# Kernel optimization log

Hardware: AMD Instinct MI355X
Metric: run time of the kernel (lower is better)

The kernel has to match this reference:

```python
import jax, jax.numpy as jnp
import numpy as np

N_NODES = 100000


def gcn_conv(x, W, b, src, dst, n_nodes):
    """PyG GCNConv: D^{-1/2} (A + I) D^{-1/2} X W + b (self loops added)."""
    xw = x @ W  # [N, F_out]
    # degree over A + I, counted on destination (col) side
    deg = jnp.zeros((n_nodes,), dtype=x.dtype).at[dst].add(1.0) + 1.0
    dinv = jax.lax.rsqrt(deg)  # deg >= 1, safe
    # edge messages with symmetric normalization
    coef = dinv[src] * dinv[dst]  # [E]
    msg = xw[src] * coef[:, None]  # [E, F_out]
    agg = jax.ops.segment_sum(msg, dst, num_segments=n_nodes)
    # self-loop contribution: dinv[i]^2 * xw[i]
    out = agg + xw * (dinv * dinv)[:, None]
    return out + b


def setup_inputs() -> dict:
    key = jax.random.key(0)
    k1, k2, k3, k4 = jax.random.split(key, 4)
    input_dim, hidden_dim, output_dim = 64, 64, 32
    n_edges = 1600000
    x = jax.random.normal(k1, (N_NODES, input_dim), dtype=jnp.float32)
    edge_index = jax.random.randint(k2, (2, n_edges), 0, N_NODES, dtype=jnp.int64)
    # Glorot-style init for GCN weights, zero bias (PyG default)
    s1 = (6.0 / (input_dim + hidden_dim)) ** 0.5
    s2 = (6.0 / (hidden_dim + output_dim)) ** 0.5
    W1 = jax.random.uniform(k3, (input_dim, hidden_dim), jnp.float32, -s1, s1)
    W2 = jax.random.uniform(k4, (hidden_dim, output_dim), jnp.float32, -s2, s2)
    b1 = jnp.zeros((hidden_dim,), jnp.float32)
    b2 = jnp.zeros((output_dim,), jnp.float32)
    return {"x": x, "edge_index": edge_index, "W1": W1, "b1": b1, "W2": W2, "b2": b2}


def reference(x, edge_index, W1, b1, W2, b2):
    src, dst = edge_index[0], edge_index[1]
    h = jax.nn.relu(gcn_conv(x, W1, b1, src, dst, N_NODES))
    return gcn_conv(h, W2, b2, src, dst, N_NODES)
```

## Files before the change

### kernel.cpp

```cpp
#include <hip/hip_runtime.h>
#include <hip/hip_fp16.h>

#define NPB   64
#define KMAX  1600
#define BCAP  1280
#define EPB   8192

typedef _Float16 f16x8 __attribute__((ext_vector_type(8)));
typedef float    f32x4 __attribute__((ext_vector_type(4)));

__global__ __launch_bounds__(256) void bucket_scatter(
    const int* __restrict__ src, const int* __restrict__ dst, int E, int K,
    int* __restrict__ bucket_fill, unsigned* __restrict__ bucket_edges) {
    __shared__ int hist[KMAX];
    __shared__ int base[KMAX];
    for (int i = threadIdx.x; i < K; i += 256) hist[i] = 0;
    __syncthreads();
    int e0 = blockIdx.x * EPB;
    int e1 = min(e0 + EPB, E);
    for (int e = e0 + threadIdx.x; e < e1; e += 256)
        atomicAdd(&hist[dst[e] >> 6], 1);
    __syncthreads();
    for (int b = threadIdx.x; b < K; b += 256) {
        int h = hist[b];
        base[b] = h ? atomicAdd(&bucket_fill[b], h) : 0;
    }
    __syncthreads();
    for (int e = e0 + threadIdx.x; e < e1; e += 256) {
        int d = dst[e];
        int bb = d >> 6;
        int pos = atomicAdd(&base[bb], 1);
        if (pos < BCAP)
            bucket_edges[(size_t)bb * BCAP + pos] =
                ((unsigned)(d & 63) << 17) | (unsigned)src[e];
    }
}

__global__ __launch_bounds__(256) void bucket_csr(
    const int* __restrict__ bucket_fill, const unsigned* __restrict__ bucket_edges,
    unsigned* __restrict__ csr, int* __restrict__ rowstart, int* __restrict__ deg,
    float* __restrict__ dinv, int N) {
    __shared__ unsigned list[BCAP];
    __shared__ int cnt[NPB], pref[NPB], cnt2[NPB];
    const int b = blockIdx.x;
    const int m = min(bucket_fill[b], BCAP);
    if (threadIdx.x < NPB) { cnt[threadIdx.x] = 0; cnt2[threadIdx.x] = 0; }
    __syncthreads();
    const unsigned* bep = bucket_edges + (size_t)b * BCAP;
    for (int e = threadIdx.x; e < m; e += 256) {
        unsigned pk = bep[e];
        list[e] = pk;
        atomicAdd(&cnt[pk >> 17], 1);
    }
    __syncthreads();
    if (threadIdx.x < 64) {
        int lane = threadIdx.x;
        int c = cnt[lane];
        int x = c;
        for (int d = 1; d < 64; d <<= 1) {
            int y = __shfl_up(x, d, 64);
            if (lane >= d) x += y;
        }
        pref[lane] = x - c;
        int g = b * NPB + lane;
        if (g < N) {
            deg[g] = c;
            rowstart[g] = b * BCAP + (x - c);
            dinv[g] = rsqrtf((float)c + 1.0f);
        }
    }
    __syncthreads();
    for (int e = threadIdx.x; e < m; e += 256) {
        unsigned pk = list[e];
        int dl = pk >> 17;
        int r = atomicAdd(&cnt2[dl], 1);
        csr[(size_t)b * BCAP + pref[dl] + r] = pk & 0x1FFFF;
    }
}

__global__ void wtrans_k(const float* __restrict__ W1, const float* __restrict__ W2,
                         __half* __restrict__ W1T, __half* __restrict__ W2T) {
    int t = threadIdx.x;
    for (int i = t; i < 64 * 64; i += 256) {
        int f = i >> 6, k = i & 63;
        W1T[i] = __float2half(W1[k * 64 + f]);
    }
    for (int i = t; i < 32 * 64; i += 256) {
        int f = i >> 6, k = i & 63;
        W2T[i] = __float2half(W2[k * 32 + f]);
    }
}

__global__ __launch_bounds__(256) void gemm1_mfma(
    const float* __restrict__ X, const __half* __restrict__ W1T,
    const float* __restrict__ dinv, __half* __restrict__ out, int N) {
    const int wave = threadIdx.x >> 6, lane = threadIdx.x & 63;
    const int r = lane & 15, q = lane >> 4;
    const int nb = blockIdx.x * 16;
    const int node = nb + r;
    const int col = wave * 16 + r;
    f32x4 acc = {0.f, 0.f, 0.f, 0.f};
#pragma unroll
    for (int kt = 0; kt < 2; ++kt) {
        const float4* xr = (const float4*)(X + (size_t)node * 64 + kt * 32 + q * 8);
        float4 p0 = xr[0], p1 = xr[1];
        f16x8 a;
        a[0] = (_Float16)p0.x; a[1] = (_Float16)p0.y; a[2] = (_Float16)p0.z; a[3] = (_Float16)p0.w;
        a[4] = (_Float16)p1.x; a[5] = (_Float16)p1.y; a[6] = (_Float16)p1.z; a[7] = (_Float16)p1.w;
        f16x8 b = *(const f16x8*)(W1T + (size_t)col * 64 + kt * 32 + q * 8);
        acc = __builtin_amdgcn_mfma_f32_16x16x32_f16(a, b, acc, 0, 0, 0);
    }
#pragma unroll
    for (int i = 0; i < 4; ++i) {
        int nd = nb + q * 4 + i;
        out[(size_t)nd * 64 + wave * 16 + r] = __float2half(acc[i] * dinv[nd]);
    }
}

__global__ __launch_bounds__(256) void gemm2_mfma(
    const __half* __restrict__ H, const __half* __restrict__ W2T,
    const float* __restrict__ dinv, __half* __restrict__ out, int N) {
    const int wave = threadIdx.x >> 6, lane = threadIdx.x & 63;
    const int r = lane & 15, q = lane >> 4;
    const int nb = blockIdx.x * 32 + (wave >> 1) * 16;
    const int cb = (wave & 1) * 16;
    const int node = nb + r;
    const int col = cb + r;
    f32x4 acc = {0.f, 0.f, 0.f, 0.f};
#pragma unroll
    for (int kt = 0; kt < 2; ++kt) {
        f16x8 a = *(const f16x8*)(H + (size_t)node * 64 + kt * 32 + q * 8);
        f16x8 b = *(const f16x8*)(W2T + (size_t)col * 64 + kt * 32 + q * 8);
        acc = __builtin_amdgcn_mfma_f32_16x16x32_f16(a, b, acc, 0, 0, 0);
    }
#pragma unroll
    for (int i = 0; i < 4; ++i) {
        int nd = nb + q * 4 + i;
        out[(size_t)nd * 32 + cb + r] = __float2half(acc[i] * dinv[nd]);
    }
}

template <int F, bool RELU, typename OT>
__global__ __launch_bounds__(256) void aggregate_h2(
    const __half* __restrict__ xws, const unsigned* __restrict__ csr,
    const int* __restrict__ rowstart, const int* __restrict__ deg,
    const float* __restrict__ dinv, const float* __restrict__ bias,
    OT* __restrict__ out, int n) {
    constexpr int LPN = F / 2;
    int t = blockIdx.x * 256 + threadIdx.x;
    int node = t / LPN;
    int fl = t % LPN;
    if (node >= n) return;
    int m = deg[node];
    const unsigned* cp = csr + rowstart[node];
    const __half2* tab = (const __half2*)xws;
    float2 acc = __half22float2(tab[(size_t)node * LPN + fl]);
    int e = 0;
    for (; e + 8 <= m; e += 8) {
        unsigned s0 = cp[e+0], s1 = cp[e+1], s2 = cp[e+2], s3 = cp[e+3];
        unsigned s4 = cp[e+4], s5 = cp[e+5], s6 = cp[e+6], s7 = cp[e+7];
        float2 a0 = __half22float2(tab[(size_t)s0 * LPN + fl]);
        float2 a1 = __half22float2(tab[(size_t)s1 * LPN + fl]);
        float2 a2 = __half22float2(tab[(size_t)s2 * LPN + fl]);
        float2 a3 = __half22float2(tab[(size_t)s3 * LPN + fl]);
        float2 a4 = __half22float2(tab[(size_t)s4 * LPN + fl]);
        float2 a5 = __half22float2(tab[(size_t)s5 * LPN + fl]);
        float2 a6 = __half22float2(tab[(size_t)s6 * LPN + fl]);
        float2 a7 = __half22float2(tab[(size_t)s7 * LPN + fl]);
        acc.x += ((a0.x + a1.x) + (a2.x + a3.x)) + ((a4.x + a5.x) + (a6.x + a7.x));
        acc.y += ((a0.y + a1.y) + (a2.y + a3.y)) + ((a4.y + a5.y) + (a6.y + a7.y));
    }
    for (; e < m; ++e) {
        float2 a = __half22float2(tab[(size_t)cp[e] * LPN + fl]);
        acc.x += a.x; acc.y += a.y;
    }
    float dn = dinv[node];
    float2 bf = ((const float2*)bias)[fl];
    float vx = acc.x * dn + bf.x;
    float vy = acc.y * dn + bf.y;
    if (RELU) { vx = fmaxf(vx, 0.f); vy = fmaxf(vy, 0.f); }
    if constexpr (sizeof(OT) == 4) {
        ((__half2*)out)[(size_t)node * LPN + fl] = __floats2half2_rn(vx, vy);
    } else {
        ((float2*)out)[(size_t)node * LPN + fl] = make_float2(vx, vy);
    }
}


extern "C" void kernel_launch(void* const* d_in, const int* in_sizes, int n_in,
                              void* d_out, int out_size, void* d_ws, size_t ws_size,
                              hipStream_t stream) {
    const float* x  = (const float*)d_in[0];
    const int*   ei = (const int*)d_in[1];
    const float* W1 = (const float*)d_in[2];
    const float* b1 = (const float*)d_in[3];
    const float* W2 = (const float*)d_in[4];
    const float* b2 = (const float*)d_in[5];
    float* out = (float*)d_out;

    const int N = in_sizes[0] / 64;
    const int E = in_sizes[1] / 2;
    const int K = (N + NPB - 1) / NPB;
    const int* src = ei;
    const int* dst = ei + E;

    unsigned* be    = (unsigned*)d_ws;
    unsigned* csr   = be + (size_t)K * BCAP;
    int*      bfill = (int*)(csr + (size_t)K * BCAP);
    int*      rowst = bfill + K;
    int*      deg   = rowst + N;
    float*    dinv  = (float*)(deg + N);
    __half*   xws   = (__half*)(dinv + N);
    __half*   h     = xws + (size_t)N * 64;
    __half*   hw2   = h + (size_t)N * 64;
    __half*   W1T   = hw2 + (size_t)N * 32;
    __half*   W2T   = W1T + 64 * 64;

    hipMemsetAsync(bfill, 0, (size_t)K * sizeof(int), stream);

    int sb = (E + EPB - 1) / EPB;
    bucket_scatter<<<sb, 256, 0, stream>>>(src, dst, E, K, bfill, be);
    wtrans_k<<<1, 256, 0, stream>>>(W1, W2, W1T, W2T);
    bucket_csr<<<K, 256, 0, stream>>>(bfill, be, csr, rowst, deg, dinv, N);

    gemm1_mfma<<<N / 16, 256, 0, stream>>>(x, W1T, dinv, xws, N);
    aggregate_h2<64, true, __half2><<<(N * 32 + 255) / 256, 256, 0, stream>>>(
        xws, csr, rowst, deg, dinv, b1, (__half2*)h, N);
    gemm2_mfma<<<N / 32, 256, 0, stream>>>(h, W2T, dinv, hw2, N);
    aggregate_h2<32, false, float2><<<(N * 16 + 255) / 256, 256, 0, stream>>>(
        hw2, csr, rowst, deg, dinv, b2, (float2*)out, N);
}
```

Before: 250.8 us.

## Locally sort edges in shared memory before bucket scatter; pad CSR rows to 8

The bucket scatter kernel now counting-sorts each block's edges by bucket in shared memory and then writes them to global memory in contiguous runs, rather than issuing scattered per-edge writes. The CSR rows are padded to multiples of 8 with a dummy index that points at an extra zero row in the feature tables, so the aggregate loop no longer needs a scalar tail. In exchange it uses much more shared memory per scatter block (about 48KB), which lowers occupancy, and the padding adds wasted gathers from the zero row.

```diff
diff --git a/kernel.cpp b/kernel.cpp
--- a/kernel.cpp
+++ b/kernel.cpp
@@ -3,7 +3,8 @@
 
 #define NPB   64
 #define KMAX  1600
-#define BCAP  1280
+#define BCAP  1408
+#define CCAP  1920
 #define EPB   8192
 
 typedef _Float16 f16x8 __attribute__((ext_vector_type(8)));
@@ -13,33 +14,60 @@
     const int* __restrict__ src, const int* __restrict__ dst, int E, int K,
     int* __restrict__ bucket_fill, unsigned* __restrict__ bucket_edges) {
     __shared__ int hist[KMAX];
-    __shared__ int base[KMAX];
-    for (int i = threadIdx.x; i < K; i += 256) hist[i] = 0;
-    __syncthreads();
-    int e0 = blockIdx.x * EPB;
-    int e1 = min(e0 + EPB, E);
-    for (int e = e0 + threadIdx.x; e < e1; e += 256)
-        atomicAdd(&hist[dst[e] >> 6], 1);
-    __syncthreads();
-    for (int b = threadIdx.x; b < K; b += 256) {
-        int h = hist[b];
-        base[b] = h ? atomicAdd(&bucket_fill[b], h) : 0;
-    }
-    __syncthreads();
-    for (int e = e0 + threadIdx.x; e < e1; e += 256) {
-        int d = dst[e];
-        int bb = d >> 6;
-        int pos = atomicAdd(&base[bb], 1);
-        if (pos < BCAP)
-            bucket_edges[(size_t)bb * BCAP + pos] =
-                ((unsigned)(d & 63) << 17) | (unsigned)src[e];
+    __shared__ int lbase[KMAX];
+    __shared__ int gbase[KMAX];
+    __shared__ unsigned sorted[EPB];
+    __shared__ unsigned short bid[EPB];
+    __shared__ int wsum[4];
+    const int t = threadIdx.x;
+    for (int i = t; i < K; i += 256) hist[i] = 0;
+    __syncthreads();
+    const int e0 = blockIdx.x * EPB;
+    const int m = min(EPB, E - e0);
+    for (int e = t; e < m; e += 256) atomicAdd(&hist[dst[e0 + e] >> 6], 1);
+    __syncthreads();
+    constexpr int CH = (KMAX + 255) / 256;
+    int c[CH]; int s = 0;
+#pragma unroll
+    for (int j = 0; j < CH; ++j) { int idx = t * CH + j; c[j] = (idx < K) ? hist[idx] : 0; s += c[j]; }
+    int lane = t & 63, w = t >> 6;
+    int x = s;
+    for (int d = 1; d < 64; d <<= 1) { int y = __shfl_up(x, d, 64); if (lane >= d) x += y; }
+    if (lane == 63) wsum[w] = x;
+    __syncthreads();
+    int run = x - s;
+    for (int j = 0; j < 4; ++j) if (j < w) run += wsum[j];
+#pragma unroll
+    for (int j = 0; j < CH; ++j) {
+        int idx = t * CH + j;
+        if (idx < K) {
+            lbase[idx] = run;
+            if (c[j] > 0) gbase[idx] = atomicAdd(&bucket_fill[idx], c[j]);
+            run += c[j];
+        }
+    }
+    __syncthreads();
+    for (int i = t; i < K; i += 256) hist[i] = 0;
+    __syncthreads();
+    for (int e = t; e < m; e += 256) {
+        int d = dst[e0 + e], b = d >> 6;
+        int r = atomicAdd(&hist[b], 1);
+        int pos = lbase[b] + r;
+        sorted[pos] = ((unsigned)(d & 63) << 17) | (unsigned)src[e0 + e];
+        bid[pos] = (unsigned short)b;
+    }
+    __syncthreads();
+    for (int i = t; i < m; i += 256) {
+        int b = bid[i];
+        int off = gbase[b] + (i - lbase[b]);
+        if (off < BCAP) bucket_edges[(size_t)b * BCAP + off] = sorted[i];
     }
 }
 
 __global__ __launch_bounds__(256) void bucket_csr(
     const int* __restrict__ bucket_fill, const unsigned* __restrict__ bucket_edges,
     unsigned* __restrict__ csr, int* __restrict__ rowstart, int* __restrict__ deg,
-    float* __restrict__ dinv, int N) {
+    float* __restrict__ dinv, int N, unsigned PAD) {
     __shared__ unsigned list[BCAP];
     __shared__ int cnt[NPB], pref[NPB], cnt2[NPB];
     const int b = blockIdx.x;
@@ -56,17 +84,23 @@
     if (threadIdx.x < 64) {
         int lane = threadIdx.x;
         int c = cnt[lane];
-        int x = c;
+        int cpad = (c + 7) & ~7;
+        int x = cpad;
         for (int d = 1; d < 64; d <<= 1) {
             int y = __shfl_up(x, d, 64);
             if (lane >= d) x += y;
         }
-        pref[lane] = x - c;
+        int ex = x - cpad;
+        pref[lane] = ex;
         int g = b * NPB + lane;
         if (g < N) {
             deg[g] = c;
-            rowstart[g] = b * BCAP + (x - c);
+            rowstart[g] = b * CCAP + ex;
             dinv[g] = rsqrtf((float)c + 1.0f);
+        }
+        for (int p = c; p < cpad; ++p) {
+            int ci = ex + p;
+            if (ci < CCAP) csr[(size_t)b * CCAP + ci] = PAD;
         }
     }
     __syncthreads();
@@ -74,7 +108,8 @@
         unsigned pk = list[e];
         int dl = pk >> 17;
         int r = atomicAdd(&cnt2[dl], 1);
-        csr[(size_t)b * BCAP + pref[dl] + r] = pk & 0x1FFFF;
+        int ci = pref[dl] + r;
+        if (ci < CCAP) csr[(size_t)b * CCAP + ci] = pk & 0x1FFFF;
     }
 }
 
@@ -151,12 +186,11 @@
     int node = t / LPN;
     int fl = t % LPN;
     if (node >= n) return;
-    int m = deg[node];
+    int mp = (deg[node] + 7) & ~7;
     const unsigned* cp = csr + rowstart[node];
     const __half2* tab = (const __half2*)xws;
     float2 acc = __half22float2(tab[(size_t)node * LPN + fl]);
-    int e = 0;
-    for (; e + 8 <= m; e += 8) {
+    for (int e = 0; e < mp; e += 8) {
         unsigned s0 = cp[e+0], s1 = cp[e+1], s2 = cp[e+2], s3 = cp[e+3];
         unsigned s4 = cp[e+4], s5 = cp[e+5], s6 = cp[e+6], s7 = cp[e+7];
         float2 a0 = __half22float2(tab[(size_t)s0 * LPN + fl]);
@@ -170,10 +204,6 @@
         acc.x += ((a0.x + a1.x) + (a2.x + a3.x)) + ((a4.x + a5.x) + (a6.x + a7.x));
         acc.y += ((a0.y + a1.y) + (a2.y + a3.y)) + ((a4.y + a5.y) + (a6.y + a7.y));
     }
-    for (; e < m; ++e) {
-        float2 a = __half22float2(tab[(size_t)cp[e] * LPN + fl]);
-        acc.x += a.x; acc.y += a.y;
-    }
     float dn = dinv[node];
     float2 bf = ((const float2*)bias)[fl];
     float vx = acc.x * dn + bf.x;
@@ -206,22 +236,24 @@
 
     unsigned* be    = (unsigned*)d_ws;
     unsigned* csr   = be + (size_t)K * BCAP;
-    int*      bfill = (int*)(csr + (size_t)K * BCAP);
+    int*      bfill = (int*)(csr + (size_t)K * CCAP);
     int*      rowst = bfill + K;
     int*      deg   = rowst + N;
     float*    dinv  = (float*)(deg + N);
     __half*   xws   = (__half*)(dinv + N);
-    __half*   h     = xws + (size_t)N * 64;
+    __half*   h     = xws + (size_t)(N + 1) * 64;
     __half*   hw2   = h + (size_t)N * 64;
-    __half*   W1T   = hw2 + (size_t)N * 32;
+    __half*   W1T   = hw2 + (size_t)(N + 1) * 32;
     __half*   W2T   = W1T + 64 * 64;
 
     hipMemsetAsync(bfill, 0, (size_t)K * sizeof(int), stream);
+    hipMemsetAsync(xws + (size_t)N * 64, 0, 64 * sizeof(__half), stream);
+    hipMemsetAsync(hw2 + (size_t)N * 32, 0, 32 * sizeof(__half), stream);
 
     int sb = (E + EPB - 1) / EPB;
     bucket_scatter<<<sb, 256, 0, stream>>>(src, dst, E, K, bfill, be);
     wtrans_k<<<1, 256, 0, stream>>>(W1, W2, W1T, W2T);
-    bucket_csr<<<K, 256, 0, stream>>>(bfill, be, csr, rowst, deg, dinv, N);
+    bucket_csr<<<K, 256, 0, stream>>>(bfill, be, csr, rowst, deg, dinv, N, (unsigned)N);
 
     gemm1_mfma<<<N / 16, 256, 0, stream>>>(x, W1T, dinv, xws, N);
     aggregate_h2<64, true, __half2><<<(N * 32 + 255) / 256, 256, 0, stream>>>(
```

New measurement: 266.7 us. 1.06x slower.
